# Kernel optimization log

Measured on AMD Instinct MI355X. Metric: run time of the kernel, lower is better.

The kernel has to match this reference:

```python
import jax, jax.numpy as jnp
import numpy as np

MARGIN = 0.3
EPS = 1e-6  # torch TripletMarginLoss pairwise_distance eps


def setup_inputs() -> dict:
    key = jax.random.key(0)
    k1, k2 = jax.random.split(key)
    n, d = 8192, 128
    inputs = jax.random.normal(k1, (n, d), dtype=jnp.float32)
    similarity = jax.random.randint(k2, (n, n), 0, 2, dtype=jnp.int32)
    return {"inputs": inputs, "similarity": similarity}


def reference(inputs, similarity):
    # mask[i, j] = True if j is a positive of anchor i
    mask = similarity != 0                      # (n, n) bool
    maskf = mask.astype(inputs.dtype)
    counts = maskf.sum(axis=1, keepdims=True)   # (n, 1), >0 by construction
    # per-anchor center = mean of its positives (masked mean as a GEMM)
    centers = (maskf @ inputs) / counts         # (n, d)
    # dist[i, j] = ||centers[i] - inputs[j]||_2 via the expansion trick
    # (avoids materializing the (n, n, d) difference tensor of the original)
    c2 = jnp.sum(centers * centers, axis=1)[:, None]
    x2 = jnp.sum(inputs * inputs, axis=1)[None, :]
    d2 = c2 + x2 - 2.0 * (centers @ inputs.T)
    dist = jnp.sqrt(jnp.maximum(d2, 0.0))       # (n, n)
    # dist only feeds argmin in the original (indices carry no grad)
    dist = jax.lax.stop_gradient(dist)
    # hard-negative mining: argmin of dist over negatives of each anchor
    neg_idx = jnp.argmin(jnp.where(mask, jnp.inf, dist), axis=1)  # (n,)
    neg_min = inputs[neg_idx]                   # (n, d)
    # TripletMarginLoss(margin=0.3, p=2): anchor=centers, pos=inputs, neg=neg_min
    d_ap = jnp.linalg.norm(centers - inputs + EPS, axis=1)
    d_an = jnp.linalg.norm(centers - neg_min + EPS, axis=1)
    return jnp.mean(jnp.maximum(d_ap - d_an + MARGIN, 0.0))
```

## Files before the change

kernel.cpp:

```cpp
#include <hip/hip_runtime.h>
#include <stdint.h>

#define NN 8192
#define DD 128

typedef float f32x4 __attribute__((ext_vector_type(4)));
typedef short bf16x8 __attribute__((ext_vector_type(8)));

union B8 { uint32_t u[4]; bf16x8 v; };

__device__ inline uint16_t f2bf(float f) {
  uint32_t u = __builtin_bit_cast(uint32_t, f);
  uint32_t r = (u + 0x7FFFu + ((u >> 16) & 1u)) >> 16;
  return (uint16_t)r;
}

__device__ inline f32x4 mfma16(bf16x8 a, bf16x8 b, f32x4 c) {
  return __builtin_amdgcn_mfma_f32_16x16x32_bf16(a, b, c, 0, 0, 0);
}

__global__ __launch_bounds__(256) void k_prep(const float* __restrict__ inp,
                                              uint16_t* __restrict__ inp_bf,
                                              uint16_t* __restrict__ inpT_bf,
                                              float* __restrict__ x2p,
                                              uint32_t* __restrict__ counts,
                                              uint32_t* __restrict__ negkey,
                                              float* __restrict__ out) {
  __shared__ uint16_t ldsT[128 * 65];
  __shared__ float ldsS[256];
  const int tid = threadIdx.x;
  const int gid = blockIdx.x * 256 + tid;
  if (gid < NN) { counts[gid] = 0u; negkey[gid] = 0xFFFFFFFFu; }
  if (gid == 0) out[0] = 0.f;
  const int j0 = blockIdx.x * 64;
  const int r = tid >> 2;
  const int dseg = (tid & 3) * 32;
  float ss = 0.f;
#pragma unroll
  for (int it = 0; it < 8; ++it) {
    float4 v = *(const float4*)(inp + (size_t)(j0 + r) * DD + dseg + it * 4);
    ss += v.x * v.x + v.y * v.y + v.z * v.z + v.w * v.w;
    uint16_t b0 = f2bf(v.x), b1 = f2bf(v.y), b2 = f2bf(v.z), b3 = f2bf(v.w);
    *(ushort4*)(inp_bf + (size_t)(j0 + r) * DD + dseg + it * 4) = make_ushort4(b0, b1, b2, b3);
    int d = dseg + it * 4;
    ldsT[(d + 0) * 65 + r] = b0;
    ldsT[(d + 1) * 65 + r] = b1;
    ldsT[(d + 2) * 65 + r] = b2;
    ldsT[(d + 3) * 65 + r] = b3;
  }
  ldsS[tid] = ss;
  __syncthreads();
  if (tid < 64)
    x2p[j0 + tid] = ldsS[tid * 4] + ldsS[tid * 4 + 1] + ldsS[tid * 4 + 2] + ldsS[tid * 4 + 3] + 512.0f;
#pragma unroll
  for (int it = 0; it < 32; ++it) {
    int flat = it * 256 + tid;
    int d = flat >> 6, jl = flat & 63;
    inpT_bf[(size_t)d * NN + j0 + jl] = ldsT[d * 65 + jl];
  }
}

__global__ __launch_bounds__(256, 2) void k_bitgen(const int* __restrict__ sim,
                                                   uint32_t* __restrict__ bmT,
                                                   uint32_t* __restrict__ counts) {
  __shared__ uint32_t ldsW[64 * 64];
  const int tid = threadIdx.x, lane = tid & 63, w = tid >> 6;
  const int m0 = blockIdx.x * 64;
  const int c0 = blockIdx.y * 2048;
  int va[32], vb[32];
  {
    const int* p = sim + (size_t)(m0 + w) * NN + c0 + lane;
#pragma unroll
    for (int s = 0; s < 32; ++s) va[s] = p[s * 64];
  }
#pragma unroll 1
  for (int rr = 0; rr < 16; ++rr) {
    const int rl = rr * 4 + w;
    if (rr < 15) {
      const int* p = sim + (size_t)(m0 + rl + 4) * NN + c0 + lane;
#pragma unroll
      for (int s = 0; s < 32; ++s) vb[s] = p[s * 64];
    }
    uint32_t cnt = 0;
#pragma unroll
    for (int s = 0; s < 32; ++s) {
      unsigned long long ball = __ballot(va[s] != 0);
      cnt += (uint32_t)__popcll(ball);
      if ((lane & 31) == 0)
        ldsW[(s * 2 + (lane >> 5)) * 64 + rl] = (uint32_t)(ball >> (lane & 32));
    }
    if (lane == 0) atomicAdd(&counts[m0 + rl], cnt);
#pragma unroll
    for (int s = 0; s < 32; ++s) va[s] = vb[s];
  }
  __syncthreads();
#pragma unroll
  for (int it = 0; it < 16; ++it) {
    int idx = it * 256 + tid;
    int kw = idx >> 6, r = idx & 63;
    bmT[(size_t)((c0 >> 5) + kw) * NN + m0 + r] = ldsW[idx];
  }
}

__global__ __launch_bounds__(256, 4) void k_gemm1(const uint16_t* __restrict__ inpT,
                                                  const uint32_t* __restrict__ bmT,
                                                  float* __restrict__ part) {
  __shared__ __align__(16) uint16_t ldsB[128 * 72];
  __shared__ uint32_t ldsM[128];
  const int tid = threadIdx.x, lane = tid & 63, w = tid >> 6;
  const int col = lane & 15, quad = lane >> 4;
  const int m0 = blockIdx.x * 64;
  const int kb0 = blockIdx.y * 1024;
  const int wm = (w >> 1) * 32, wn = (w & 1) * 64;
  const int dim = tid >> 1, koff = (tid & 1) * 32;
  const int mrow = tid >> 1, msel = tid & 1;
  f32x4 acc[2][4];
  const f32x4 z = {0.f, 0.f, 0.f, 0.f};
#pragma unroll
  for (int r = 0; r < 2; ++r)
#pragma unroll
    for (int c = 0; c < 4; ++c) acc[r][c] = z;

  bf16x8 bpf[4];
#pragma unroll
  for (int it = 0; it < 4; ++it)
    bpf[it] = *(const bf16x8*)(inpT + (size_t)dim * NN + kb0 + koff + it * 8);
  uint32_t mpf = (tid < 128) ? bmT[(size_t)((kb0 >> 5) + msel) * NN + m0 + mrow] : 0u;

  for (int ks = 0; ks < 16; ++ks) {
    const int kb = kb0 + ks * 64;
    __syncthreads();
#pragma unroll
    for (int it = 0; it < 4; ++it)
      *(bf16x8*)(ldsB + dim * 72 + koff + it * 8) = bpf[it];
    if (tid < 128) ldsM[mrow * 2 + msel] = mpf;
    __syncthreads();
    if (ks < 15) {
#pragma unroll
      for (int it = 0; it < 4; ++it)
        bpf[it] = *(const bf16x8*)(inpT + (size_t)dim * NN + kb + 64 + koff + it * 8);
      if (tid < 128) mpf = bmT[(size_t)(((kb + 64) >> 5) + msel) * NN + m0 + mrow];
    }
#pragma unroll
    for (int h = 0; h < 2; ++h) {
      B8 af[2];
#pragma unroll
      for (int rr = 0; rr < 2; ++rr) {
        uint32_t word = ldsM[(wm + rr * 16 + col) * 2 + h];
        uint32_t b = (word >> (quad * 8)) & 0xFFu;
        uint32_t s = b * 0x8001u;
#pragma unroll
        for (int p = 0; p < 4; ++p) {
          uint32_t t = (s >> (2 * p)) & 0x10001u;
          af[rr].u[p] = t * 0x3F80u;
        }
      }
#pragma unroll
      for (int cc = 0; cc < 4; ++cc) {
        bf16x8 bfr = *(const bf16x8*)(ldsB + (wn + cc * 16 + col) * 72 + h * 32 + quad * 8);
#pragma unroll
        for (int rr = 0; rr < 2; ++rr) acc[rr][cc] = mfma16(af[rr].v, bfr, acc[rr][cc]);
      }
    }
  }
  float* pp = part + (size_t)blockIdx.y * NN * DD;
#pragma unroll
  for (int rr = 0; rr < 2; ++rr)
#pragma unroll
    for (int cc = 0; cc < 4; ++cc)
#pragma unroll
      for (int g = 0; g < 4; ++g)
        pp[(size_t)(m0 + wm + rr * 16 + quad * 4 + g) * DD + wn + cc * 16 + col] = acc[rr][cc][g];
}

__global__ __launch_bounds__(256) void k_reduce(const float* __restrict__ part,
                                                const uint32_t* __restrict__ counts,
                                                float* __restrict__ centers,
                                                uint16_t* __restrict__ cen_bf) {
  const int gid = blockIdx.x * 256 + threadIdx.x;
  const int idx = gid * 4;
  const int row = idx >> 7;
  const float inv = 1.0f / (float)counts[row];
  float4 v = *(const float4*)(part + idx);
#pragma unroll
  for (int s = 1; s < 8; ++s) {
    float4 u = *(const float4*)(part + (size_t)s * NN * DD + idx);
    v.x += u.x; v.y += u.y; v.z += u.z; v.w += u.w;
  }
  v.x *= inv; v.y *= inv; v.z *= inv; v.w *= inv;
  *(float4*)(centers + idx) = v;
  *(ushort4*)(cen_bf + idx) = make_ushort4(f2bf(v.x), f2bf(v.y), f2bf(v.z), f2bf(v.w));
}

__global__ __launch_bounds__(256, 4) void k_argmin(const uint16_t* __restrict__ cen_bf,
                                                   const uint16_t* __restrict__ inp_bf,
                                                   const uint32_t* __restrict__ bmT,
                                                   const float* __restrict__ x2p,
                                                   uint32_t* __restrict__ negkey) {
  __shared__ __align__(16) uint16_t ldsB[64 * 136];
  __shared__ uint32_t ldsM[128];
  __shared__ float ldsX[64];
  __shared__ uint32_t ldsR[64];
  const int tid = threadIdx.x, lane = tid & 63, w = tid >> 6;
  const int col = lane & 15, quad = lane >> 4;
  const int i0 = blockIdx.x * 64;
  const int jbase = blockIdx.y * 1024;
  const int wi = (w >> 1) * 32, wj = (w & 1) * 32;
  bf16x8 af[2][4];
#pragma unroll
  for (int rr = 0; rr < 2; ++rr)
#pragma unroll
    for (int kk = 0; kk < 4; ++kk)
      af[rr][kk] = *(const bf16x8*)(cen_bf + (size_t)(i0 + wi + rr * 16 + col) * DD + kk * 32 + quad * 8);
  if (tid < 64) ldsR[tid] = 0xFFFFFFFFu;
  uint32_t best[2][4];
#pragma unroll
  for (int rr = 0; rr < 2; ++rr)
#pragma unroll
    for (int g = 0; g < 4; ++g) best[rr][g] = 0xFFFFFFFFu;

  const int jl = tid >> 2, doff = (tid & 3) * 32;
  bf16x8 bpf[4];
#pragma unroll
  for (int it = 0; it < 4; ++it)
    bpf[it] = *(const bf16x8*)(inp_bf + (size_t)(jbase + jl) * DD + doff + it * 8);
  uint32_t mpf = (tid < 128) ? bmT[(size_t)((jbase >> 5) + (tid >> 6)) * NN + i0 + (tid & 63)] : 0u;
  float xpf = (tid >= 128 && tid < 192) ? x2p[jbase + tid - 128] : 0.f;

  for (int js = 0; js < 16; ++js) {
    const int j0 = jbase + js * 64;
    __syncthreads();
#pragma unroll
    for (int it = 0; it < 4; ++it)
      *(bf16x8*)(ldsB + jl * 136 + doff + it * 8) = bpf[it];
    if (tid < 128) ldsM[tid] = mpf;
    else if (tid < 192) ldsX[tid - 128] = xpf;
    __syncthreads();
    if (js < 15) {
#pragma unroll
      for (int it = 0; it < 4; ++it)
        bpf[it] = *(const bf16x8*)(inp_bf + (size_t)(j0 + 64 + jl) * DD + doff + it * 8);
      if (tid < 128) mpf = bmT[(size_t)(((j0 + 64) >> 5) + (tid >> 6)) * NN + i0 + (tid & 63)];
      else if (tid < 192) xpf = x2p[j0 + 64 + tid - 128];
    }
    f32x4 acc[2][2];
    const f32x4 z = {0.f, 0.f, 0.f, 0.f};
    acc[0][0] = z; acc[0][1] = z; acc[1][0] = z; acc[1][1] = z;
#pragma unroll
    for (int kk = 0; kk < 4; ++kk) {
      bf16x8 b0 = *(const bf16x8*)(ldsB + (wj + col) * 136 + kk * 32 + quad * 8);
      bf16x8 b1 = *(const bf16x8*)(ldsB + (wj + 16 + col) * 136 + kk * 32 + quad * 8);
      acc[0][0] = mfma16(af[0][kk], b0, acc[0][0]);
      acc[0][1] = mfma16(af[0][kk], b1, acc[0][1]);
      acc[1][0] = mfma16(af[1][kk], b0, acc[1][0]);
      acc[1][1] = mfma16(af[1][kk], b1, acc[1][1]);
    }
    const uint32_t wsel = (w & 1) * 64;
    uint32_t words[2][4];
#pragma unroll
    for (int rr = 0; rr < 2; ++rr)
#pragma unroll
      for (int g = 0; g < 4; ++g) words[rr][g] = ldsM[wsel + wi + rr * 16 + quad * 4 + g];
#pragma unroll
    for (int cc = 0; cc < 2; ++cc) {
      const int jj = wj + cc * 16 + col;
      const float xq = ldsX[jj];
      const uint32_t jpre = (uint32_t)(j0 + jj);
      const int sh = 31 - (cc * 16 + col);
#pragma unroll
      for (int rr = 0; rr < 2; ++rr)
#pragma unroll
        for (int g = 0; g < 4; ++g) {
          float v = fmaf(-2.0f, acc[rr][cc][g], xq);
          uint32_t u = __builtin_bit_cast(uint32_t, v);
          uint32_t key = (u & 0xFFFFE000u) | jpre;
          key |= (words[rr][g] << sh) & 0x80000000u;
          best[rr][g] = min(best[rr][g], key);
        }
    }
  }
#pragma unroll
  for (int rr = 0; rr < 2; ++rr)
#pragma unroll
    for (int g = 0; g < 4; ++g) {
      uint32_t k = best[rr][g];
#pragma unroll
      for (int d = 1; d < 16; d <<= 1) {
        uint32_t o = (uint32_t)__shfl_xor((int)k, d);
        k = min(k, o);
      }
      if (col == 0) atomicMin(&ldsR[wi + rr * 16 + quad * 4 + g], k);
    }
  __syncthreads();
  if (tid < 64) atomicMin(&negkey[i0 + tid], ldsR[tid]);
}

__global__ __launch_bounds__(256) void k_loss(const float* __restrict__ centers,
                                              const float* __restrict__ inp,
                                              const uint32_t* __restrict__ negkey,
                                              float* __restrict__ out) {
  __shared__ float lds[4];
  const int tid = threadIdx.x, lane = tid & 63, w = tid >> 6;
  float local = 0.f;
#pragma unroll 1
  for (int a = 0; a < 4; ++a) {
    int i = blockIdx.x * 16 + w * 4 + a;
    float2 c = *(const float2*)(centers + (size_t)i * DD + lane * 2);
    float2 x = *(const float2*)(inp + (size_t)i * DD + lane * 2);
    uint32_t ni = negkey[i] & (NN - 1);
    float2 gv = *(const float2*)(inp + (size_t)ni * DD + lane * 2);
    float e0 = c.x - x.x + 1e-6f, e1 = c.y - x.y + 1e-6f;
    float f0 = c.x - gv.x + 1e-6f, f1 = c.y - gv.y + 1e-6f;
    float dap = e0 * e0 + e1 * e1;
    float dan = f0 * f0 + f1 * f1;
#pragma unroll
    for (int d = 32; d; d >>= 1) {
      dap += __shfl_down(dap, d);
      dan += __shfl_down(dan, d);
    }
    if (lane == 0) local += fmaxf(sqrtf(dap) - sqrtf(dan) + 0.3f, 0.f);
  }
  if (lane == 0) lds[w] = local;
  __syncthreads();
  if (tid == 0) atomicAdd(out, (lds[0] + lds[1] + lds[2] + lds[3]) * (1.0f / 8192.0f));
}

extern "C" void kernel_launch(void* const* d_in, const int* in_sizes, int n_in,
                              void* d_out, int out_size, void* d_ws, size_t ws_size,
                              hipStream_t stream) {
  (void)in_sizes; (void)n_in; (void)out_size; (void)ws_size;
  const float* inp = (const float*)d_in[0];
  const int* sim = (const int*)d_in[1];
  float* out = (float*)d_out;
  char* ws = (char*)d_ws;

  uint32_t* bmT     = (uint32_t*)ws;
  float* part       = (float*)(ws + (8u << 20));
  float* centers    = (float*)(ws + (40u << 20));
  uint16_t* inp_bf  = (uint16_t*)(ws + (44u << 20));
  uint16_t* inpT_bf = (uint16_t*)(ws + (46u << 20));
  uint16_t* cen_bf  = (uint16_t*)(ws + (48u << 20));
  float* x2p        = (float*)(ws + (50u << 20));
  uint32_t* counts  = (uint32_t*)(ws + (50u << 20) + 32768u);
  uint32_t* negkey  = (uint32_t*)(ws + (50u << 20) + 65536u);

  k_prep<<<128, 256, 0, stream>>>(inp, inp_bf, inpT_bf, x2p, counts, negkey, out);
  k_bitgen<<<dim3(128, 4), 256, 0, stream>>>(sim, bmT, counts);
  k_gemm1<<<dim3(128, 8), 256, 0, stream>>>(inpT_bf, bmT, part);
  k_reduce<<<1024, 256, 0, stream>>>(part, counts, centers, cen_bf);
  k_argmin<<<dim3(128, 8), 256, 0, stream>>>(cen_bf, inp_bf, bmT, x2p, negkey);
  k_loss<<<512, 256, 0, stream>>>(centers, inp, negkey, out);
}
```

Baseline: 446.0 us.

## Drop LDS staging in gemm1 and argmin, load MFMA fragments directly with register double-buffering

Both GEMM-like kernels stop staging B-tiles and mask words through shared memory. Each wave now loads its MFMA operand fragments straight from global memory into registers, double-buffered (A/B sets) so loads overlap compute, and __syncthreads barriers are removed. Tiles grow to 128 rows per block, which halves the grid and lowers the occupancy hint to 2. Argmin now does atomicMin directly to global instead of reducing through LDS first. The cost is more redundant global/L2 traffic, since waves no longer share loads, plus higher register pressure.

```diff
diff --git a/kernel.cpp b/kernel.cpp
--- a/kernel.cpp
+++ b/kernel.cpp
@@ -102,70 +102,69 @@
   }
 }
 
-__global__ __launch_bounds__(256, 4) void k_gemm1(const uint16_t* __restrict__ inpT,
+__global__ __launch_bounds__(256, 2) void k_gemm1(const uint16_t* __restrict__ inpT,
                                                   const uint32_t* __restrict__ bmT,
                                                   float* __restrict__ part) {
-  __shared__ __align__(16) uint16_t ldsB[128 * 72];
-  __shared__ uint32_t ldsM[128];
   const int tid = threadIdx.x, lane = tid & 63, w = tid >> 6;
   const int col = lane & 15, quad = lane >> 4;
-  const int m0 = blockIdx.x * 64;
+  const int m0 = blockIdx.x * 128;
   const int kb0 = blockIdx.y * 1024;
-  const int wm = (w >> 1) * 32, wn = (w & 1) * 64;
-  const int dim = tid >> 1, koff = (tid & 1) * 32;
-  const int mrow = tid >> 1, msel = tid & 1;
-  f32x4 acc[2][4];
+  const int wm = (w >> 1) * 64, wn = (w & 1) * 64;
+  f32x4 acc[4][4];
   const f32x4 z = {0.f, 0.f, 0.f, 0.f};
 #pragma unroll
-  for (int r = 0; r < 2; ++r)
+  for (int r = 0; r < 4; ++r)
 #pragma unroll
     for (int c = 0; c < 4; ++c) acc[r][c] = z;
 
-  bf16x8 bpf[4];
-#pragma unroll
-  for (int it = 0; it < 4; ++it)
-    bpf[it] = *(const bf16x8*)(inpT + (size_t)dim * NN + kb0 + koff + it * 8);
-  uint32_t mpf = (tid < 128) ? bmT[(size_t)((kb0 >> 5) + msel) * NN + m0 + mrow] : 0u;
-
-  for (int ks = 0; ks < 16; ++ks) {
+  bf16x8 bpA[8], bpB[8];
+  uint32_t mwA[8], mwB[8];
+
+#define LOADK(BP, MW, KB)                                                                     \
+  {                                                                                           \
+    _Pragma("unroll") for (int cc = 0; cc < 4; ++cc)                                          \
+      _Pragma("unroll") for (int h = 0; h < 2; ++h)                                           \
+        BP[cc * 2 + h] =                                                                      \
+            *(const bf16x8*)(inpT + (size_t)(wn + cc * 16 + col) * NN + (KB) + h * 32 + quad * 8); \
+    _Pragma("unroll") for (int rr = 0; rr < 4; ++rr)                                          \
+      _Pragma("unroll") for (int h = 0; h < 2; ++h)                                           \
+        MW[rr * 2 + h] = bmT[(size_t)(((KB) >> 5) + h) * NN + m0 + wm + rr * 16 + col];       \
+  }
+
+#define STEPK(BP, MW)                                                                         \
+  {                                                                                           \
+    _Pragma("unroll") for (int h = 0; h < 2; ++h) {                                           \
+      B8 af[4];                                                                               \
+      _Pragma("unroll") for (int rr = 0; rr < 4; ++rr) {                                      \
+        uint32_t word = MW[rr * 2 + h];                                                       \
+        uint32_t b = (word >> (quad * 8)) & 0xFFu;                                            \
+        uint32_t s = b * 0x8001u;                                                             \
+        _Pragma("unroll") for (int p = 0; p < 4; ++p)                                         \
+          af[rr].u[p] = ((s >> (2 * p)) & 0x10001u) * 0x3F80u;                                \
+      }                                                                                       \
+      _Pragma("unroll") for (int cc = 0; cc < 4; ++cc) {                                      \
+        bf16x8 bfr = BP[cc * 2 + h];                                                          \
+        _Pragma("unroll") for (int rr = 0; rr < 4; ++rr)                                      \
+          acc[rr][cc] = mfma16(af[rr].v, bfr, acc[rr][cc]);                                   \
+      }                                                                                       \
+    }                                                                                         \
+  }
+
+  LOADK(bpA, mwA, kb0);
+#pragma unroll 1
+  for (int ks = 0; ks < 16; ks += 2) {
     const int kb = kb0 + ks * 64;
-    __syncthreads();
-#pragma unroll
-    for (int it = 0; it < 4; ++it)
-      *(bf16x8*)(ldsB + dim * 72 + koff + it * 8) = bpf[it];
-    if (tid < 128) ldsM[mrow * 2 + msel] = mpf;
-    __syncthreads();
-    if (ks < 15) {
-#pragma unroll
-      for (int it = 0; it < 4; ++it)
-        bpf[it] = *(const bf16x8*)(inpT + (size_t)dim * NN + kb + 64 + koff + it * 8);
-      if (tid < 128) mpf = bmT[(size_t)(((kb + 64) >> 5) + msel) * NN + m0 + mrow];
-    }
-#pragma unroll
-    for (int h = 0; h < 2; ++h) {
-      B8 af[2];
-#pragma unroll
-      for (int rr = 0; rr < 2; ++rr) {
-        uint32_t word = ldsM[(wm + rr * 16 + col) * 2 + h];
-        uint32_t b = (word >> (quad * 8)) & 0xFFu;
-        uint32_t s = b * 0x8001u;
-#pragma unroll
-        for (int p = 0; p < 4; ++p) {
-          uint32_t t = (s >> (2 * p)) & 0x10001u;
-          af[rr].u[p] = t * 0x3F80u;
-        }
-      }
-#pragma unroll
-      for (int cc = 0; cc < 4; ++cc) {
-        bf16x8 bfr = *(const bf16x8*)(ldsB + (wn + cc * 16 + col) * 72 + h * 32 + quad * 8);
-#pragma unroll
-        for (int rr = 0; rr < 2; ++rr) acc[rr][cc] = mfma16(af[rr].v, bfr, acc[rr][cc]);
-      }
-    }
-  }
+    LOADK(bpB, mwB, kb + 64);
+    STEPK(bpA, mwA);
+    if (ks + 2 < 16) LOADK(bpA, mwA, kb + 128);
+    STEPK(bpB, mwB);
+  }
+#undef LOADK
+#undef STEPK
+
   float* pp = part + (size_t)blockIdx.y * NN * DD;
 #pragma unroll
-  for (int rr = 0; rr < 2; ++rr)
+  for (int rr = 0; rr < 4; ++rr)
 #pragma unroll
     for (int cc = 0; cc < 4; ++cc)
 #pragma unroll
@@ -192,93 +191,86 @@
   *(ushort4*)(cen_bf + idx) = make_ushort4(f2bf(v.x), f2bf(v.y), f2bf(v.z), f2bf(v.w));
 }
 
-__global__ __launch_bounds__(256, 4) void k_argmin(const uint16_t* __restrict__ cen_bf,
+__global__ __launch_bounds__(256, 2) void k_argmin(const uint16_t* __restrict__ cen_bf,
                                                    const uint16_t* __restrict__ inp_bf,
                                                    const uint32_t* __restrict__ bmT,
                                                    const float* __restrict__ x2p,
                                                    uint32_t* __restrict__ negkey) {
-  __shared__ __align__(16) uint16_t ldsB[64 * 136];
-  __shared__ uint32_t ldsM[128];
-  __shared__ float ldsX[64];
-  __shared__ uint32_t ldsR[64];
   const int tid = threadIdx.x, lane = tid & 63, w = tid >> 6;
   const int col = lane & 15, quad = lane >> 4;
-  const int i0 = blockIdx.x * 64;
+  const int i0 = blockIdx.x * 128;
   const int jbase = blockIdx.y * 1024;
-  const int wi = (w >> 1) * 32, wj = (w & 1) * 32;
+  const int wi = w * 32;
+
   bf16x8 af[2][4];
 #pragma unroll
   for (int rr = 0; rr < 2; ++rr)
 #pragma unroll
     for (int kk = 0; kk < 4; ++kk)
       af[rr][kk] = *(const bf16x8*)(cen_bf + (size_t)(i0 + wi + rr * 16 + col) * DD + kk * 32 + quad * 8);
-  if (tid < 64) ldsR[tid] = 0xFFFFFFFFu;
+
   uint32_t best[2][4];
 #pragma unroll
   for (int rr = 0; rr < 2; ++rr)
 #pragma unroll
     for (int g = 0; g < 4; ++g) best[rr][g] = 0xFFFFFFFFu;
 
-  const int jl = tid >> 2, doff = (tid & 3) * 32;
-  bf16x8 bpf[4];
-#pragma unroll
-  for (int it = 0; it < 4; ++it)
-    bpf[it] = *(const bf16x8*)(inp_bf + (size_t)(jbase + jl) * DD + doff + it * 8);
-  uint32_t mpf = (tid < 128) ? bmT[(size_t)((jbase >> 5) + (tid >> 6)) * NN + i0 + (tid & 63)] : 0u;
-  float xpf = (tid >= 128 && tid < 192) ? x2p[jbase + tid - 128] : 0.f;
-
-  for (int js = 0; js < 16; ++js) {
-    const int j0 = jbase + js * 64;
-    __syncthreads();
-#pragma unroll
-    for (int it = 0; it < 4; ++it)
-      *(bf16x8*)(ldsB + jl * 136 + doff + it * 8) = bpf[it];
-    if (tid < 128) ldsM[tid] = mpf;
-    else if (tid < 192) ldsX[tid - 128] = xpf;
-    __syncthreads();
-    if (js < 15) {
-#pragma unroll
-      for (int it = 0; it < 4; ++it)
-        bpf[it] = *(const bf16x8*)(inp_bf + (size_t)(j0 + 64 + jl) * DD + doff + it * 8);
-      if (tid < 128) mpf = bmT[(size_t)(((j0 + 64) >> 5) + (tid >> 6)) * NN + i0 + (tid & 63)];
-      else if (tid < 192) xpf = x2p[j0 + 64 + tid - 128];
-    }
-    f32x4 acc[2][2];
-    const f32x4 z = {0.f, 0.f, 0.f, 0.f};
-    acc[0][0] = z; acc[0][1] = z; acc[1][0] = z; acc[1][1] = z;
-#pragma unroll
-    for (int kk = 0; kk < 4; ++kk) {
-      bf16x8 b0 = *(const bf16x8*)(ldsB + (wj + col) * 136 + kk * 32 + quad * 8);
-      bf16x8 b1 = *(const bf16x8*)(ldsB + (wj + 16 + col) * 136 + kk * 32 + quad * 8);
-      acc[0][0] = mfma16(af[0][kk], b0, acc[0][0]);
-      acc[0][1] = mfma16(af[0][kk], b1, acc[0][1]);
-      acc[1][0] = mfma16(af[1][kk], b0, acc[1][0]);
-      acc[1][1] = mfma16(af[1][kk], b1, acc[1][1]);
-    }
-    const uint32_t wsel = (w & 1) * 64;
-    uint32_t words[2][4];
-#pragma unroll
-    for (int rr = 0; rr < 2; ++rr)
-#pragma unroll
-      for (int g = 0; g < 4; ++g) words[rr][g] = ldsM[wsel + wi + rr * 16 + quad * 4 + g];
-#pragma unroll
-    for (int cc = 0; cc < 2; ++cc) {
-      const int jj = wj + cc * 16 + col;
-      const float xq = ldsX[jj];
-      const uint32_t jpre = (uint32_t)(j0 + jj);
-      const int sh = 31 - (cc * 16 + col);
-#pragma unroll
-      for (int rr = 0; rr < 2; ++rr)
-#pragma unroll
-        for (int g = 0; g < 4; ++g) {
-          float v = fmaf(-2.0f, acc[rr][cc][g], xq);
-          uint32_t u = __builtin_bit_cast(uint32_t, v);
-          uint32_t key = (u & 0xFFFFE000u) | jpre;
-          key |= (words[rr][g] << sh) & 0x80000000u;
-          best[rr][g] = min(best[rr][g], key);
-        }
-    }
-  }
+  const f32x4 z = {0.f, 0.f, 0.f, 0.f};
+  bf16x8 bpA[8], bpB[8];
+  uint32_t mwA[8], mwB[8];
+  float xvA[2], xvB[2];
+
+#define LOADJ(BP, MW, XV, J0)                                                                 \
+  {                                                                                           \
+    _Pragma("unroll") for (int cc = 0; cc < 2; ++cc)                                          \
+      _Pragma("unroll") for (int kk = 0; kk < 4; ++kk)                                        \
+        BP[cc * 4 + kk] =                                                                     \
+            *(const bf16x8*)(inp_bf + (size_t)((J0) + cc * 16 + col) * DD + kk * 32 + quad * 8); \
+    _Pragma("unroll") for (int rr = 0; rr < 2; ++rr)                                          \
+      _Pragma("unroll") for (int g = 0; g < 4; ++g)                                           \
+        MW[rr * 4 + g] = bmT[(size_t)((J0) >> 5) * NN + i0 + wi + rr * 16 + quad * 4 + g];    \
+    _Pragma("unroll") for (int cc = 0; cc < 2; ++cc) XV[cc] = x2p[(J0) + cc * 16 + col];      \
+  }
+
+#define STEPJ(BP, MW, XV, J0)                                                                 \
+  {                                                                                           \
+    f32x4 acc[2][2];                                                                          \
+    acc[0][0] = z; acc[0][1] = z; acc[1][0] = z; acc[1][1] = z;                               \
+    _Pragma("unroll") for (int kk = 0; kk < 4; ++kk) {                                        \
+      bf16x8 b0 = BP[kk];                                                                     \
+      bf16x8 b1 = BP[4 + kk];                                                                 \
+      acc[0][0] = mfma16(af[0][kk], b0, acc[0][0]);                                           \
+      acc[0][1] = mfma16(af[0][kk], b1, acc[0][1]);                                           \
+      acc[1][0] = mfma16(af[1][kk], b0, acc[1][0]);                                           \
+      acc[1][1] = mfma16(af[1][kk], b1, acc[1][1]);                                           \
+    }                                                                                         \
+    _Pragma("unroll") for (int cc = 0; cc < 2; ++cc) {                                        \
+      const float xq = XV[cc];                                                                \
+      const uint32_t jpre = (uint32_t)((J0) + cc * 16 + col);                                 \
+      const int sh = 31 - (cc * 16 + col);                                                    \
+      _Pragma("unroll") for (int rr = 0; rr < 2; ++rr)                                        \
+        _Pragma("unroll") for (int g = 0; g < 4; ++g) {                                       \
+          float v = fmaf(-2.0f, acc[rr][cc][g], xq);                                          \
+          uint32_t u = __builtin_bit_cast(uint32_t, v);                                       \
+          uint32_t key = (u & 0xFFFFE000u) | jpre;                                            \
+          key |= (MW[rr * 4 + g] << sh) & 0x80000000u;                                        \
+          best[rr][g] = min(best[rr][g], key);                                                \
+        }                                                                                     \
+    }                                                                                         \
+  }
+
+  LOADJ(bpA, mwA, xvA, jbase);
+#pragma unroll 1
+  for (int st = 0; st < 32; st += 2) {
+    const int j0 = jbase + st * 32;
+    LOADJ(bpB, mwB, xvB, j0 + 32);
+    STEPJ(bpA, mwA, xvA, j0);
+    if (st + 2 < 32) LOADJ(bpA, mwA, xvA, j0 + 64);
+    STEPJ(bpB, mwB, xvB, j0 + 32);
+  }
+#undef LOADJ
+#undef STEPJ
+
 #pragma unroll
   for (int rr = 0; rr < 2; ++rr)
 #pragma unroll
@@ -289,10 +281,8 @@
         uint32_t o = (uint32_t)__shfl_xor((int)k, d);
         k = min(k, o);
       }
-      if (col == 0) atomicMin(&ldsR[wi + rr * 16 + quad * 4 + g], k);
+      if (col == 0) atomicMin(&negkey[i0 + wi + rr * 16 + quad * 4 + g], k);
     }
-  __syncthreads();
-  if (tid < 64) atomicMin(&negkey[i0 + tid], ldsR[tid]);
 }
 
 __global__ __launch_bounds__(256) void k_loss(const float* __restrict__ centers,
@@ -346,8 +336,8 @@
 
   k_prep<<<128, 256, 0, stream>>>(inp, inp_bf, inpT_bf, x2p, counts, negkey, out);
   k_bitgen<<<dim3(128, 4), 256, 0, stream>>>(sim, bmT, counts);
-  k_gemm1<<<dim3(128, 8), 256, 0, stream>>>(inpT_bf, bmT, part);
+  k_gemm1<<<dim3(64, 8), 256, 0, stream>>>(inpT_bf, bmT, part);
   k_reduce<<<1024, 256, 0, stream>>>(part, counts, centers, cen_bf);
-  k_argmin<<<dim3(128, 8), 256, 0, stream>>>(cen_bf, inp_bf, bmT, x2p, negkey);
+  k_argmin<<<dim3(64, 8), 256, 0, stream>>>(cen_bf, inp_bf, bmT, x2p, negkey);
   k_loss<<<512, 256, 0, stream>>>(centers, inp, negkey, out);
 }
```

Measured after the change: 490.1 us. 1.1x slower.
